# Performance work log

Measured on AMD Instinct MI355X. Metric: run time of the kernel, lower is better.

## Reference

```python
import jax, jax.numpy as jnp
import numpy as np

VAD_TH_GT = 2.0 / 3.0
VAD_TH_EST = 2.0 / 3.0
AE_TH = 30.0
DEG2RAD = np.pi / 180.0
CLIP = 0.99999


def setup_inputs() -> dict:
    key = jax.random.key(0)
    k1, k2, k3, k4 = jax.random.split(key, 4)
    nb, nt, ns = 64, 16384, 4
    # DOAs in degrees: row 0 = elevation [0,180], row 1 = azimuth [0,360]
    doa_gt = jax.random.uniform(k1, (nb, nt, 2, ns), dtype=jnp.float32)
    doa_gt = doa_gt * jnp.array([180.0, 360.0], dtype=jnp.float32)[None, None, :, None]
    doa_est = jax.random.uniform(k2, (nb, nt, 2, ns), dtype=jnp.float32)
    doa_est = doa_est * jnp.array([180.0, 360.0], dtype=jnp.float32)[None, None, :, None]
    vad_gt = jax.random.uniform(k3, (nb, nt, ns), dtype=jnp.float32)
    vad_est = jax.random.uniform(k4, (nb, nt, ns), dtype=jnp.float32)
    return {"doa_gt": doa_gt, "vad_gt": vad_gt, "doa_est": doa_est, "vad_est": vad_est}


def _angular_errors(doa_est, doa_gt):
    # doa_*: (nb, nt, 2, ns); index 0 = ele, index 1 = azi (degrees)
    azi_err = jnp.abs(jnp.mod(doa_est[:, :, 1, :] - doa_gt[:, :, 1, :] + 180.0, 360.0) - 180.0)
    ele_err = jnp.abs(doa_est[:, :, 0, :] - doa_gt[:, :, 0, :])
    ele_gt = doa_gt[:, :, 0, :] * DEG2RAD
    azi_gt = doa_gt[:, :, 1, :] * DEG2RAD
    ele_es = doa_est[:, :, 0, :] * DEG2RAD
    azi_es = doa_est[:, :, 1, :] * DEG2RAD
    aux = jnp.cos(ele_gt) * jnp.cos(ele_es) + jnp.sin(ele_gt) * jnp.sin(ele_es) * jnp.cos(azi_gt - azi_es)
    aux = jnp.clip(aux, -CLIP, CLIP)
    aziele_err = jnp.abs(jnp.arccos(aux)) / DEG2RAD
    return azi_err, ele_err, aziele_err


def reference(doa_gt, vad_gt, doa_est, vad_est):
    # source_mode='single', useVAD=True, ae_mode=['ele','azi','aziele']
    vg = (vad_gt > VAD_TH_GT).astype(jnp.float32)   # act flag
    ve = (vad_est > VAD_TH_EST).astype(jnp.float32) * vg
    azi_err, ele_err, aziele_err = _angular_errors(doa_est, doa_gt)
    corr_flag = (azi_err < AE_TH).astype(jnp.float32) * ve
    act_sum = jnp.sum(vg)
    ACC = jnp.sum(corr_flag) / act_sum
    MAE = jnp.stack([
        jnp.sum(vg * ele_err) / act_sum,     # 'ele'
        jnp.sum(vg * azi_err) / act_sum,     # 'azi'
        jnp.sum(vg * aziele_err) / act_sum,  # 'aziele'
    ])
    return ACC, MAE
```

## Files before the change

kernel.cpp:

```cpp
#include <hip/hip_runtime.h>
#include <math.h>

namespace {

constexpr int NB = 64, NT = 16384;
constexpr int NBT = NB * NT;
constexpr int NBLK   = 2048;
constexpr int NTHR   = 256;
constexpr int NPASS  = NBT / (NBLK * NTHR);
constexpr float VAD_TH  = 2.0f / 3.0f;
constexpr float AE_TH   = 30.0f;
constexpr float D2R     = 0.017453292519943295f;
constexpr float R2D     = 57.29577951308232f;
constexpr float CLIPV   = 0.99999f;


__device__ __forceinline__ void process4(
    const float4& eg, const float4& ag, const float4& ee, const float4& ae,
    const float4& vg4, const float4& ve4,
    float& act, float& corr, float& s_ele, float& s_azi, float& s_ae)
{
    float egA[4] = {eg.x, eg.y, eg.z, eg.w}, agA[4] = {ag.x, ag.y, ag.z, ag.w};
    float eeA[4] = {ee.x, ee.y, ee.z, ee.w}, aeA[4] = {ae.x, ae.y, ae.z, ae.w};
    float vgA[4] = {vg4.x, vg4.y, vg4.z, vg4.w}, veA[4] = {ve4.x, ve4.y, ve4.z, ve4.w};

#pragma unroll
    for (int s = 0; s < 4; ++s) {
        float vg = (vgA[s] > VAD_TH) ? 1.f : 0.f;
        float ve = (veA[s] > VAD_TH) ? vg : 0.f;

        float d = aeA[s] - agA[s] + 180.f;
        d = (d < 0.f) ? d + 360.f : d;
        d = (d >= 360.f) ? d - 360.f : d;
        float azi_err = fabsf(d - 180.f);

        float ele_err = fabsf(eeA[s] - egA[s]);

        float gr = egA[s] * D2R;
        float er = eeA[s] * D2R;
        float ar = agA[s] * D2R - aeA[s] * D2R;
        float aux = __cosf(gr) * __cosf(er) + __sinf(gr) * __sinf(er) * __cosf(ar);
        aux = fminf(fmaxf(aux, -CLIPV), CLIPV);
        float ae_err = acosf(aux) * R2D;

        act += vg;
        if (azi_err < AE_TH) corr += ve;
        s_ele += vg * ele_err;
        s_azi += vg * azi_err;
        s_ae  += vg * ae_err;
    }
}

__global__ __launch_bounds__(NTHR) void metric_main(
    const float* __restrict__ doa_gt, const float* __restrict__ vad_gt,
    const float* __restrict__ doa_est, const float* __restrict__ vad_est,
    float* __restrict__ part)
{
    const int gid = blockIdx.x * NTHR + threadIdx.x;

    const float4* dg = reinterpret_cast<const float4*>(doa_gt);
    const float4* de = reinterpret_cast<const float4*>(doa_est);
    const float4* vg_p = reinterpret_cast<const float4*>(vad_gt);
    const float4* ve_p = reinterpret_cast<const float4*>(vad_est);

    const int i0 = gid;
    const int i1 = gid + NBLK * NTHR;
    static_assert(NPASS == 2, "load schedule assumes 2 passes");

    float4 eg0 = dg[2 * i0], ag0 = dg[2 * i0 + 1];
    float4 ee0 = de[2 * i0], ae0 = de[2 * i0 + 1];
    float4 eg1 = dg[2 * i1], ag1 = dg[2 * i1 + 1];
    float4 ee1 = de[2 * i1], ae1 = de[2 * i1 + 1];
    float4 vg40 = vg_p[i0], ve40 = ve_p[i0];
    float4 vg41 = vg_p[i1], ve41 = ve_p[i1];

    float act = 0.f, corr = 0.f, s_ele = 0.f, s_azi = 0.f, s_ae = 0.f;
    process4(eg0, ag0, ee0, ae0, vg40, ve40, act, corr, s_ele, s_azi, s_ae);
    process4(eg1, ag1, ee1, ae1, vg41, ve41, act, corr, s_ele, s_azi, s_ae);

#pragma unroll
    for (int off = 32; off > 0; off >>= 1) {
        act   += __shfl_down(act,   off, 64);
        corr  += __shfl_down(corr,  off, 64);
        s_ele += __shfl_down(s_ele, off, 64);
        s_azi += __shfl_down(s_azi, off, 64);
        s_ae  += __shfl_down(s_ae,  off, 64);
    }

    __shared__ float sm[4][5];
    const int wave = threadIdx.x >> 6;
    const int lane = threadIdx.x & 63;
    if (lane == 0) {
        sm[wave][0] = act;  sm[wave][1] = corr; sm[wave][2] = s_ele;
        sm[wave][3] = s_azi; sm[wave][4] = s_ae;
    }
    __syncthreads();
    if (threadIdx.x == 0) {
        part[0 * NBLK + blockIdx.x] = sm[0][0] + sm[1][0] + sm[2][0] + sm[3][0];
        part[1 * NBLK + blockIdx.x] = sm[0][1] + sm[1][1] + sm[2][1] + sm[3][1];
        part[2 * NBLK + blockIdx.x] = sm[0][2] + sm[1][2] + sm[2][2] + sm[3][2];
        part[3 * NBLK + blockIdx.x] = sm[0][3] + sm[1][3] + sm[2][3] + sm[3][3];
        part[4 * NBLK + blockIdx.x] = sm[0][4] + sm[1][4] + sm[2][4] + sm[3][4];
    }
}

__global__ __launch_bounds__(NTHR) void metric_finalize(
    const float* __restrict__ part, float* __restrict__ out)
{
    __shared__ double dsm[4][5];
    const int t = threadIdx.x;
    double v[5];
#pragma unroll
    for (int m = 0; m < 5; ++m) {
        double acc = 0.0;
#pragma unroll
        for (int j = 0; j < NBLK / NTHR; ++j)
            acc += (double)part[m * NBLK + j * NTHR + t];
        v[m] = acc;
    }
#pragma unroll
    for (int off = 32; off > 0; off >>= 1)
#pragma unroll
        for (int m = 0; m < 5; ++m)
            v[m] += __shfl_down(v[m], off, 64);

    const int wave = t >> 6, lane = t & 63;
    if (lane == 0)
#pragma unroll
        for (int m = 0; m < 5; ++m) dsm[wave][m] = v[m];
    __syncthreads();
    if (t == 0) {
        double tot[5];
#pragma unroll
        for (int m = 0; m < 5; ++m)
            tot[m] = dsm[0][m] + dsm[1][m] + dsm[2][m] + dsm[3][m];
        double act = tot[0];
        out[0] = (float)(tot[1] / act);
        out[1] = (float)(tot[2] / act);
        out[2] = (float)(tot[3] / act);
        out[3] = (float)(tot[4] / act);
    }
}

}

extern "C" void kernel_launch(void* const* d_in, const int* in_sizes, int n_in,
                              void* d_out, int out_size, void* d_ws, size_t ws_size,
                              hipStream_t stream) {
    const float* doa_gt  = (const float*)d_in[0];
    const float* vad_gt  = (const float*)d_in[1];
    const float* doa_est = (const float*)d_in[2];
    const float* vad_est = (const float*)d_in[3];
    float* part = (float*)d_ws;
    float* out  = (float*)d_out;

    metric_main<<<NBLK, NTHR, 0, stream>>>(doa_gt, vad_gt, doa_est, vad_est, part);
    metric_finalize<<<1, NTHR, 0, stream>>>(part, out);
}
```

Baseline: 119.1 us.

## Fuse finalize into main kernel via last-block atomic and use nontemporal loads

Merges the separate finalize launch into the main reduction kernel: each block publishes its partials, increments an atomic counter, and the last block to arrive performs the double-precision final reduction. A memset of the counter replaces the second kernel launch. All input loads switch to nontemporal builtins on ext_vector float4 types, to reduce cache pollution from the streaming read. The memset still adds a stream operation, and the fence/atomic adds a little per-block overhead.

```diff
diff --git a/kernel.cpp b/kernel.cpp
--- a/kernel.cpp
+++ b/kernel.cpp
@@ -15,30 +15,32 @@
 constexpr float CLIPV   = 0.99999f;
 
 
+typedef float f32x4 __attribute__((ext_vector_type(4)));
+
+__device__ __forceinline__ f32x4 ntld(const f32x4* __restrict__ p) {
+    return __builtin_nontemporal_load(p);
+}
+
 __device__ __forceinline__ void process4(
-    const float4& eg, const float4& ag, const float4& ee, const float4& ae,
-    const float4& vg4, const float4& ve4,
+    const f32x4 eg, const f32x4 ag, const f32x4 ee, const f32x4 ae,
+    const f32x4 vg4, const f32x4 ve4,
     float& act, float& corr, float& s_ele, float& s_azi, float& s_ae)
 {
-    float egA[4] = {eg.x, eg.y, eg.z, eg.w}, agA[4] = {ag.x, ag.y, ag.z, ag.w};
-    float eeA[4] = {ee.x, ee.y, ee.z, ee.w}, aeA[4] = {ae.x, ae.y, ae.z, ae.w};
-    float vgA[4] = {vg4.x, vg4.y, vg4.z, vg4.w}, veA[4] = {ve4.x, ve4.y, ve4.z, ve4.w};
-
 #pragma unroll
     for (int s = 0; s < 4; ++s) {
-        float vg = (vgA[s] > VAD_TH) ? 1.f : 0.f;
-        float ve = (veA[s] > VAD_TH) ? vg : 0.f;
+        float vg = (vg4[s] > VAD_TH) ? 1.f : 0.f;
+        float ve = (ve4[s] > VAD_TH) ? vg : 0.f;
 
-        float d = aeA[s] - agA[s] + 180.f;
+        float d = ae[s] - ag[s] + 180.f;
         d = (d < 0.f) ? d + 360.f : d;
         d = (d >= 360.f) ? d - 360.f : d;
         float azi_err = fabsf(d - 180.f);
 
-        float ele_err = fabsf(eeA[s] - egA[s]);
+        float ele_err = fabsf(ee[s] - eg[s]);
 
-        float gr = egA[s] * D2R;
-        float er = eeA[s] * D2R;
-        float ar = agA[s] * D2R - aeA[s] * D2R;
+        float gr = eg[s] * D2R;
+        float er = ee[s] * D2R;
+        float ar = ag[s] * D2R - ae[s] * D2R;
         float aux = __cosf(gr) * __cosf(er) + __sinf(gr) * __sinf(er) * __cosf(ar);
         aux = fminf(fmaxf(aux, -CLIPV), CLIPV);
         float ae_err = acosf(aux) * R2D;
@@ -54,25 +56,26 @@
 __global__ __launch_bounds__(NTHR) void metric_main(
     const float* __restrict__ doa_gt, const float* __restrict__ vad_gt,
     const float* __restrict__ doa_est, const float* __restrict__ vad_est,
-    float* __restrict__ part)
+    float* __restrict__ part, unsigned* __restrict__ cnt,
+    float* __restrict__ out)
 {
     const int gid = blockIdx.x * NTHR + threadIdx.x;
 
-    const float4* dg = reinterpret_cast<const float4*>(doa_gt);
-    const float4* de = reinterpret_cast<const float4*>(doa_est);
-    const float4* vg_p = reinterpret_cast<const float4*>(vad_gt);
-    const float4* ve_p = reinterpret_cast<const float4*>(vad_est);
+    const f32x4* dg = reinterpret_cast<const f32x4*>(doa_gt);
+    const f32x4* de = reinterpret_cast<const f32x4*>(doa_est);
+    const f32x4* vg_p = reinterpret_cast<const f32x4*>(vad_gt);
+    const f32x4* ve_p = reinterpret_cast<const f32x4*>(vad_est);
 
     const int i0 = gid;
     const int i1 = gid + NBLK * NTHR;
     static_assert(NPASS == 2, "load schedule assumes 2 passes");
 
-    float4 eg0 = dg[2 * i0], ag0 = dg[2 * i0 + 1];
-    float4 ee0 = de[2 * i0], ae0 = de[2 * i0 + 1];
-    float4 eg1 = dg[2 * i1], ag1 = dg[2 * i1 + 1];
-    float4 ee1 = de[2 * i1], ae1 = de[2 * i1 + 1];
-    float4 vg40 = vg_p[i0], ve40 = ve_p[i0];
-    float4 vg41 = vg_p[i1], ve41 = ve_p[i1];
+    f32x4 eg0 = ntld(&dg[2 * i0]), ag0 = ntld(&dg[2 * i0 + 1]);
+    f32x4 ee0 = ntld(&de[2 * i0]), ae0 = ntld(&de[2 * i0 + 1]);
+    f32x4 eg1 = ntld(&dg[2 * i1]), ag1 = ntld(&dg[2 * i1 + 1]);
+    f32x4 ee1 = ntld(&de[2 * i1]), ae1 = ntld(&de[2 * i1 + 1]);
+    f32x4 vg40 = ntld(&vg_p[i0]), ve40 = ntld(&ve_p[i0]);
+    f32x4 vg41 = ntld(&vg_p[i1]), ve41 = ntld(&ve_p[i1]);
 
     float act = 0.f, corr = 0.f, s_ele = 0.f, s_azi = 0.f, s_ae = 0.f;
     process4(eg0, ag0, ee0, ae0, vg40, ve40, act, corr, s_ele, s_azi, s_ae);
@@ -88,6 +91,9 @@
     }
 
     __shared__ float sm[4][5];
+    __shared__ int   sm_last;
+    __shared__ double dsm[4][5];
+
     const int wave = threadIdx.x >> 6;
     const int lane = threadIdx.x & 63;
     if (lane == 0) {
@@ -101,13 +107,14 @@
         part[2 * NBLK + blockIdx.x] = sm[0][2] + sm[1][2] + sm[2][2] + sm[3][2];
         part[3 * NBLK + blockIdx.x] = sm[0][3] + sm[1][3] + sm[2][3] + sm[3][3];
         part[4 * NBLK + blockIdx.x] = sm[0][4] + sm[1][4] + sm[2][4] + sm[3][4];
+        __threadfence();
+        unsigned old = atomicAdd(cnt, 1u);
+        sm_last = (old == (unsigned)(NBLK - 1)) ? 1 : 0;
     }
-}
+    __syncthreads();
+    if (!sm_last) return;
 
-__global__ __launch_bounds__(NTHR) void metric_finalize(
-    const float* __restrict__ part, float* __restrict__ out)
-{
-    __shared__ double dsm[4][5];
+    __threadfence();
     const int t = threadIdx.x;
     double v[5];
 #pragma unroll
@@ -124,7 +131,6 @@
         for (int m = 0; m < 5; ++m)
             v[m] += __shfl_down(v[m], off, 64);
 
-    const int wave = t >> 6, lane = t & 63;
     if (lane == 0)
 #pragma unroll
         for (int m = 0; m < 5; ++m) dsm[wave][m] = v[m];
@@ -134,11 +140,11 @@
 #pragma unroll
         for (int m = 0; m < 5; ++m)
             tot[m] = dsm[0][m] + dsm[1][m] + dsm[2][m] + dsm[3][m];
-        double act = tot[0];
-        out[0] = (float)(tot[1] / act);
-        out[1] = (float)(tot[2] / act);
-        out[2] = (float)(tot[3] / act);
-        out[3] = (float)(tot[4] / act);
+        double act_s = tot[0];
+        out[0] = (float)(tot[1] / act_s);
+        out[1] = (float)(tot[2] / act_s);
+        out[2] = (float)(tot[3] / act_s);
+        out[3] = (float)(tot[4] / act_s);
     }
 }
 
@@ -152,8 +158,9 @@
     const float* doa_est = (const float*)d_in[2];
     const float* vad_est = (const float*)d_in[3];
     float* part = (float*)d_ws;
+    unsigned* cnt = (unsigned*)((char*)d_ws + 5 * NBLK * sizeof(float));
     float* out  = (float*)d_out;
 
-    metric_main<<<NBLK, NTHR, 0, stream>>>(doa_gt, vad_gt, doa_est, vad_est, part);
-    metric_finalize<<<1, NTHR, 0, stream>>>(part, out);
+    hipMemsetAsync(cnt, 0, sizeof(unsigned), stream);
+    metric_main<<<NBLK, NTHR, 0, stream>>>(doa_gt, vad_gt, doa_est, vad_est, part, cnt, out);
 }
```

Result: slower. 220.2 us (+84.9%).
